# Kernel optimization log

Hardware: AMD Instinct MI355X
Metric: run time of the kernel (lower is better)

## Reference

```python
import jax, jax.numpy as jnp
import numpy as np

S, H, E, DFF = 8192, 1024, 8, 4096
CAPACITY = (S * 1) // E  # capacity_factor=1.0, k=1 -> 1024 (>= min_capacity 4)


def setup_inputs() -> dict:
    key = jax.random.key(0)
    ks = jax.random.split(key, 6)
    sc_in = 1.0 / np.sqrt(H)
    sc_ff = 1.0 / np.sqrt(DFF)
    return {
        "hidden_states": jax.random.normal(ks[0], (S, H), dtype=jnp.float32),
        "wg": jax.random.normal(ks[1], (H, E), dtype=jnp.float32) * sc_in,
        "w1": jax.random.normal(ks[2], (E, H, DFF), dtype=jnp.float32) * sc_in,
        "b1": jnp.zeros((E, DFF), dtype=jnp.float32),
        "w2": jax.random.normal(ks[3], (E, DFF, H), dtype=jnp.float32) * sc_ff,
        "b2": jnp.zeros((E, H), dtype=jnp.float32),
    }


def _top1_gate(x, wg):
    # DeepSpeed top1gating (noisy_gate_policy=None, used_token=None)
    logits = x @ wg                                   # [S, E]
    gates = jax.nn.softmax(logits, axis=-1)           # [S, E]
    idx = jnp.argmax(gates, axis=-1)                  # [S]
    mask1 = jax.nn.one_hot(idx, E, dtype=gates.dtype) # [S, E]
    # load-balancing aux loss (uses pre-capacity mask)
    me = jnp.mean(gates, axis=0)
    ce = jnp.mean(mask1, axis=0)
    l_aux = jnp.sum(me * ce) * E
    # capacity-based token dropping
    locations1 = jnp.cumsum(mask1, axis=0) - 1.0      # position within expert
    mask1 = mask1 * (locations1 < CAPACITY)
    exp_counts = jnp.sum(mask1, axis=0).astype(jnp.int32)
    loc_s = jnp.sum(locations1 * mask1, axis=1).astype(jnp.int32)   # [S]
    loc_sc = jax.nn.one_hot(loc_s, CAPACITY, dtype=gates.dtype)     # [S, C]
    combine = jnp.einsum("se,sc->sec", gates * mask1, loc_sc)       # [S, E, C]
    dispatch = (combine > 0).astype(gates.dtype)
    return l_aux, combine, dispatch, exp_counts


def reference(hidden_states, wg, w1, b1, w2, b2):
    l_aux, combine, dispatch, exp_counts = _top1_gate(hidden_states, wg)
    # dispatch tokens to expert slots: [E, C, H]
    disp = jnp.einsum("sec,sh->ech", dispatch, hidden_states)
    # grouped expert FFN (GELU MLP)
    h1 = jax.nn.gelu(jnp.einsum("ech,ehf->ecf", disp, w1) + b1[:, None, :])
    eo = jnp.einsum("ecf,efh->ech", h1, w2) + b2[:, None, :]
    # combine back to token order, weighted by gate values
    out = jnp.einsum("sec,ech->sh", combine, eo)      # [S, H]
    # dropout prob = 0.0 -> identity
    return out, l_aux, exp_counts
```

## Files before the change

kernel.cpp:

```cpp
#include <hip/hip_runtime.h>

#define S_TOK 8192
#define H_DIM 1024
#define NE    8
#define CAP   1024
#define DFF   4096

typedef unsigned short u16;
typedef __bf16 bf16_t;
typedef bf16_t bf16x8 __attribute__((ext_vector_type(8)));
typedef float  f32x4  __attribute__((ext_vector_type(4)));

__device__ __forceinline__ u16 f2bf(float f) {
  union { float f; unsigned u; } a; a.f = f;
  unsigned u = a.u;
  u += 0x7fffu + ((u >> 16) & 1u);
  return (u16)(u >> 16);
}

__device__ __forceinline__ float gelu_tanh(float x) {
  const float c = 0.7978845608028654f;
  float t = tanhf(c * (x + 0.044715f * x * x * x));
  return 0.5f * x * (1.0f + t);
}

__global__ void gate_kernel(const float* __restrict__ x, const float* __restrict__ wg,
                            float* __restrict__ gate, int* __restrict__ expert,
                            int* __restrict__ rank, int* __restrict__ blockCnt,
                            float* __restrict__ blockMe) {
  __shared__ float sg[16][8];
  __shared__ int   se[16];
  int tid = threadIdx.x, lane = tid & 63, w = tid >> 6;
  int b = blockIdx.x;
  for (int j = 0; j < 4; ++j) {
    int t = w * 4 + j;
    int s = b * 16 + t;
    const float* xr = x + (size_t)s * H_DIM;
    float acc[8];
#pragma unroll
    for (int e = 0; e < 8; ++e) acc[e] = 0.f;
#pragma unroll
    for (int i = 0; i < 16; ++i) {
      int h = i * 64 + lane;
      float xv = xr[h];
      float4 wa = *(const float4*)(wg + h * 8);
      float4 wb = *(const float4*)(wg + h * 8 + 4);
      acc[0] += xv * wa.x; acc[1] += xv * wa.y; acc[2] += xv * wa.z; acc[3] += xv * wa.w;
      acc[4] += xv * wb.x; acc[5] += xv * wb.y; acc[6] += xv * wb.z; acc[7] += xv * wb.w;
    }
#pragma unroll
    for (int off = 32; off >= 1; off >>= 1)
#pragma unroll
      for (int e = 0; e < 8; ++e) acc[e] += __shfl_down(acc[e], off);
    if (lane == 0) {
      float mx = acc[0];
#pragma unroll
      for (int e = 1; e < 8; ++e) mx = fmaxf(mx, acc[e]);
      float g[8], Z = 0.f;
#pragma unroll
      for (int e = 0; e < 8; ++e) { g[e] = expf(acc[e] - mx); Z += g[e]; }
      int am = 0; float best = acc[0];
#pragma unroll
      for (int e = 1; e < 8; ++e) if (acc[e] > best) { best = acc[e]; am = e; }
      float inv = 1.f / Z;
#pragma unroll
      for (int e = 0; e < 8; ++e) sg[t][e] = g[e] * inv;
      se[t] = am;
      gate[s] = g[am] * inv;
      expert[s] = am;
    }
  }
  __syncthreads();
  if (tid < 16) {
    int e = se[tid], r = 0;
    for (int t2 = 0; t2 < tid; ++t2) r += (se[t2] == e) ? 1 : 0;
    rank[b * 16 + tid] = r;
  }
  if (tid < 8) {
    int c = 0; float m = 0.f;
#pragma unroll
    for (int t = 0; t < 16; ++t) { c += (se[t] == tid) ? 1 : 0; m += sg[t][tid]; }
    blockCnt[b * 8 + tid] = c;
    blockMe[b * 8 + tid] = m;
  }
}

__global__ void scan_kernel(const int* __restrict__ blockCnt, const float* __restrict__ blockMe,
                            int* __restrict__ blockOff, int* __restrict__ counts,
                            float* __restrict__ tail) {
  int tid = threadIdx.x;
  int e = tid >> 6, lane = tid & 63;
  int run = 0; float msum = 0.f;
  for (int c = 0; c < 8; ++c) {
    int b = c * 64 + lane;
    int v = blockCnt[b * 8 + e];
    float mv = blockMe[b * 8 + e];
    int sc = v;
#pragma unroll
    for (int off = 1; off < 64; off <<= 1) {
      int u = __shfl_up(sc, off);
      if (lane >= off) sc += u;
    }
    blockOff[b * 8 + e] = run + sc - v;
    run += __shfl(sc, 63);
#pragma unroll
    for (int off = 32; off >= 1; off >>= 1) mv += __shfl_down(mv, off);
    msum += __shfl(mv, 0);
  }
  __shared__ float sm[8];
  __shared__ int scnt[8];
  if (lane == 0) {
    sm[e] = msum; scnt[e] = run;
    counts[e] = run < CAP ? run : CAP;
  }
  __syncthreads();
  if (tid == 0) {
    float la = 0.f;
    for (int i = 0; i < 8; ++i)
      la += (sm[i] / (float)S_TOK) * ((float)scnt[i] / (float)S_TOK);
    tail[0] = la * (float)NE;
    for (int i = 0; i < 8; ++i) {
      int cc = scnt[i] < CAP ? scnt[i] : CAP;
      tail[1 + i] = (float)cc;
    }
  }
}

__global__ void assign_kernel(const int* __restrict__ expert, const int* __restrict__ rank,
                              const int* __restrict__ blockOff, int* __restrict__ slot_token) {
  int s = blockIdx.x * 256 + threadIdx.x;
  int e = expert[s];
  int pos = blockOff[(s >> 4) * 8 + e] + rank[s];
  if (pos < CAP) slot_token[e * CAP + pos] = s;
}

__global__ void gather_kernel(const float* __restrict__ x, const int* __restrict__ slot_token,
                              const int* __restrict__ counts, u16* __restrict__ disp) {
  int slot = blockIdx.x;
  int e = slot >> 10, c = slot & 1023;
  int t = threadIdx.x;
  ushort4 v4;
  if (c < counts[e]) {
    int s = slot_token[slot];
    float4 v = *(const float4*)(x + (size_t)s * H_DIM + t * 4);
    v4.x = f2bf(v.x); v4.y = f2bf(v.y); v4.z = f2bf(v.z); v4.w = f2bf(v.w);
  } else {
    v4.x = 0; v4.y = 0; v4.z = 0; v4.w = 0;
  }
  *(ushort4*)(disp + (size_t)slot * H_DIM + t * 4) = v4;
}

__global__ void transpose_convert(const float* __restrict__ src0, u16* __restrict__ dst0,
                                  int R, int C) {
  __shared__ float tile[64][65];
  int e = blockIdx.z;
  const float* src = src0 + (size_t)e * R * C;
  u16* dst = dst0 + (size_t)e * R * C;
  int c0 = blockIdx.x * 64, r0 = blockIdx.y * 64;
  int g = threadIdx.x & 15, rr = threadIdx.x >> 4;
#pragma unroll
  for (int p = 0; p < 4; ++p) {
    int r = rr + p * 16;
    float4 v = *(const float4*)(src + (size_t)(r0 + r) * C + c0 + g * 4);
    tile[r][g * 4 + 0] = v.x;
    tile[r][g * 4 + 1] = v.y;
    tile[r][g * 4 + 2] = v.z;
    tile[r][g * 4 + 3] = v.w;
  }
  __syncthreads();
#pragma unroll
  for (int p = 0; p < 4; ++p) {
    int c = rr + p * 16;
    ushort4 o;
    o.x = f2bf(tile[g * 4 + 0][c]);
    o.y = f2bf(tile[g * 4 + 1][c]);
    o.z = f2bf(tile[g * 4 + 2][c]);
    o.w = f2bf(tile[g * 4 + 3][c]);
    *(ushort4*)(dst + (size_t)(c0 + c) * R + r0 + g * 4) = o;
  }
}

__global__ __launch_bounds__(256, 2) void gemm1_kernel(const u16* __restrict__ disp,
                                                       const u16* __restrict__ w1t,
                                                       const float* __restrict__ b1,
                                                       u16* __restrict__ h1) {
  __shared__ __align__(16) u16 As[2][8192];
  __shared__ __align__(16) u16 Bs[2][8192];
  int flat = blockIdx.x;
  int swz = (flat & 7) * 256 + (flat >> 3);
  int e  = swz >> 8;
  int r  = swz & 255;
  int bx = r >> 3;
  int by = r & 7;
  int m0 = by * 128, n0 = bx * 128;
  const u16* A  = disp + (size_t)e * CAP * H_DIM + (size_t)m0 * H_DIM;
  const u16* Bt = w1t + (size_t)e * DFF * H_DIM + (size_t)n0 * H_DIM;

  int tid = threadIdx.x, lane = tid & 63, w = tid >> 6;
  int wm = w >> 1, wn = w & 1, q = lane >> 4, l15 = lane & 15;

  const u16* gpA[4]; const u16* gpB[4]; int lofs[4];
#pragma unroll
  for (int i = 0; i < 4; ++i) {
    int p = (w * 4 + i) * 64 + lane;
    int row = p >> 3, slot = p & 7;
    int kq = slot ^ (row & 7);
    gpA[i] = A + (size_t)row * H_DIM + kq * 8;
    gpB[i] = Bt + (size_t)row * H_DIM + kq * 8;
    lofs[i] = (w * 4 + i) * 512;
  }

  int aoff[2][4], boff[2][4];
#pragma unroll
  for (int t = 0; t < 4; ++t) {
    int ra = wm * 64 + t * 16 + l15;
    int rb = wn * 64 + t * 16 + l15;
#pragma unroll
    for (int s = 0; s < 2; ++s) {
      aoff[s][t] = ra * 64 + (((s * 4) + q) ^ (ra & 7)) * 8;
      boff[s][t] = rb * 64 + (((s * 4) + q) ^ (rb & 7)) * 8;
    }
  }

  f32x4 acc[4][4];
  f32x4 zero = {0.f, 0.f, 0.f, 0.f};
#pragma unroll
  for (int i = 0; i < 4; ++i)
#pragma unroll
    for (int j = 0; j < 4; ++j) acc[i][j] = zero;

#pragma unroll
  for (int i = 0; i < 4; ++i) {
    __builtin_amdgcn_global_load_lds((__attribute__((address_space(1))) int*)(gpA[i]),
                                     (__attribute__((address_space(3))) int*)(&As[0][0] + lofs[i]), 16, 0, 0);
    __builtin_amdgcn_global_load_lds((__attribute__((address_space(1))) int*)(gpB[i]),
                                     (__attribute__((address_space(3))) int*)(&Bs[0][0] + lofs[i]), 16, 0, 0);
  }
  __syncthreads();

  int cur = 0;
  for (int kt = 0; kt < H_DIM; kt += 64) {
    if (kt + 64 < H_DIM) {
      int nxt = cur ^ 1;
#pragma unroll
      for (int i = 0; i < 4; ++i) {
        __builtin_amdgcn_global_load_lds((__attribute__((address_space(1))) int*)(gpA[i] + kt + 64),
                                         (__attribute__((address_space(3))) int*)(&As[nxt][0] + lofs[i]), 16, 0, 0);
        __builtin_amdgcn_global_load_lds((__attribute__((address_space(1))) int*)(gpB[i] + kt + 64),
                                         (__attribute__((address_space(3))) int*)(&Bs[nxt][0] + lofs[i]), 16, 0, 0);
      }
    }
#pragma unroll
    for (int s = 0; s < 2; ++s) {
      bf16x8 af[4], bfr[4];
#pragma unroll
      for (int t = 0; t < 4; ++t) af[t] = *(const bf16x8*)(&As[cur][0] + aoff[s][t]);
#pragma unroll
      for (int t = 0; t < 4; ++t) bfr[t] = *(const bf16x8*)(&Bs[cur][0] + boff[s][t]);
#pragma unroll
      for (int mt = 0; mt < 4; ++mt)
#pragma unroll
        for (int nt = 0; nt < 4; ++nt)
          acc[mt][nt] = __builtin_amdgcn_mfma_f32_16x16x32_bf16(af[mt], bfr[nt], acc[mt][nt], 0, 0, 0);
    }
    __syncthreads();
    cur ^= 1;
  }

  const float* b1e = b1 + e * DFF;
  u16* out = h1 + (size_t)e * CAP * DFF;
#pragma unroll
  for (int mt = 0; mt < 4; ++mt)
#pragma unroll
    for (int nt = 0; nt < 4; ++nt) {
      int col = n0 + wn * 64 + nt * 16 + l15;
      float bias = b1e[col];
#pragma unroll
      for (int rr = 0; rr < 4; ++rr) {
        int row = m0 + wm * 64 + mt * 16 + q * 4 + rr;
        out[(size_t)row * DFF + col] = f2bf(gelu_tanh(acc[mt][nt][rr] + bias));
      }
    }
}

__global__ __launch_bounds__(512, 4) void gemm2_kernel(const u16* __restrict__ h1,
                                                       const u16* __restrict__ w2t,
                                                       const float* __restrict__ b2,
                                                       const int* __restrict__ slot_token,
                                                       const float* __restrict__ gate,
                                                       const int* __restrict__ counts,
                                                       float* __restrict__ out) {
  __shared__ __align__(16) u16 As[2][8192];
  __shared__ __align__(16) u16 Bs[2][8192];
  int flat = blockIdx.x;
  int swz = (flat & 7) * 64 + (flat >> 3);
  int e  = swz >> 6;
  int r  = swz & 63;
  int bx = r & 7;
  int by = r >> 3;
  int m0 = by * 128, n0 = bx * 128;
  const u16* A  = h1 + (size_t)e * CAP * DFF + (size_t)m0 * DFF;
  const u16* Bt = w2t + (size_t)e * H_DIM * DFF + (size_t)n0 * DFF;
  int tid = threadIdx.x, lane = tid & 63, w = tid >> 6;
  int wm = w >> 2, wn = w & 3;
  int q = lane >> 4, l15 = lane & 15;
  f32x4 acc[4][2];
  f32x4 zero = {0.f, 0.f, 0.f, 0.f};
#pragma unroll
  for (int i = 0; i < 4; ++i) { acc[i][0] = zero; acc[i][1] = zero; }

  const u16* gsrc = (w < 4) ? A : Bt;
  int isA = (w < 4) ? 1 : 0;
  int q4 = w & 3;
  const u16* gp[4]; int lofs[4];
#pragma unroll
  for (int i = 0; i < 4; ++i) {
    int p = (q4 * 4 + i) * 64 + lane;
    int row = p >> 3, slot = p & 7;
    int kq = slot ^ (row & 7);
    gp[i] = gsrc + (size_t)row * DFF + kq * 8;
    lofs[i] = (q4 * 4 + i) * 512;
  }

  int aoff[2][4], boff[2][2];
#pragma unroll
  for (int t = 0; t < 4; ++t) {
    int ra = wm * 64 + t * 16 + l15;
#pragma unroll
    for (int s = 0; s < 2; ++s)
      aoff[s][t] = ra * 64 + (((s * 4) + q) ^ (ra & 7)) * 8;
  }
#pragma unroll
  for (int t = 0; t < 2; ++t) {
    int rb = wn * 32 + t * 16 + l15;
#pragma unroll
    for (int s = 0; s < 2; ++s)
      boff[s][t] = rb * 64 + (((s * 4) + q) ^ (rb & 7)) * 8;
  }

  {
    u16* sb = isA ? &As[0][0] : &Bs[0][0];
#pragma unroll
    for (int i = 0; i < 4; ++i)
      __builtin_amdgcn_global_load_lds((__attribute__((address_space(1))) int*)(gp[i]),
                                       (__attribute__((address_space(3))) int*)(sb + lofs[i]), 16, 0, 0);
  }
  __syncthreads();

  int cur = 0;
  for (int kt = 0; kt < DFF; kt += 64) {
    if (kt + 64 < DFF) {
      int nxt = cur ^ 1;
      u16* sb = isA ? &As[nxt][0] : &Bs[nxt][0];
#pragma unroll
      for (int i = 0; i < 4; ++i)
        __builtin_amdgcn_global_load_lds((__attribute__((address_space(1))) int*)(gp[i] + kt + 64),
                                         (__attribute__((address_space(3))) int*)(sb + lofs[i]), 16, 0, 0);
    }
#pragma unroll
    for (int s = 0; s < 2; ++s) {
      bf16x8 af[4], bfr[2];
#pragma unroll
      for (int t = 0; t < 4; ++t) af[t] = *(const bf16x8*)(&As[cur][0] + aoff[s][t]);
#pragma unroll
      for (int t = 0; t < 2; ++t) bfr[t] = *(const bf16x8*)(&Bs[cur][0] + boff[s][t]);
#pragma unroll
      for (int mt = 0; mt < 4; ++mt)
#pragma unroll
        for (int nt = 0; nt < 2; ++nt)
          acc[mt][nt] = __builtin_amdgcn_mfma_f32_16x16x32_bf16(af[mt], bfr[nt], acc[mt][nt], 0, 0, 0);
    }
    __syncthreads();
    cur ^= 1;
  }

  int cnt = counts[e];
  const float* b2e = b2 + e * H_DIM;
#pragma unroll
  for (int mt = 0; mt < 4; ++mt) {
    int tok[4]; float gv[4];
#pragma unroll
    for (int rr = 0; rr < 4; ++rr) {
      int c = m0 + wm * 64 + mt * 16 + q * 4 + rr;
      if (c < cnt) { int s = slot_token[e * CAP + c]; tok[rr] = s; gv[rr] = gate[s]; }
      else { tok[rr] = -1; gv[rr] = 0.f; }
    }
#pragma unroll
    for (int nt = 0; nt < 2; ++nt) {
      int col = n0 + wn * 32 + nt * 16 + l15;
      float bias = b2e[col];
#pragma unroll
      for (int rr = 0; rr < 4; ++rr)
        if (tok[rr] >= 0)
          out[(size_t)tok[rr] * H_DIM + col] = gv[rr] * (acc[mt][nt][rr] + bias);
    }
  }
}

extern "C" void kernel_launch(void* const* d_in, const int* in_sizes, int n_in,
                              void* d_out, int out_size, void* d_ws, size_t ws_size,
                              hipStream_t stream) {
  const float* x  = (const float*)d_in[0];
  const float* wg = (const float*)d_in[1];
  const float* w1 = (const float*)d_in[2];
  const float* b1 = (const float*)d_in[3];
  const float* w2 = (const float*)d_in[4];
  const float* b2 = (const float*)d_in[5];
  float* out = (float*)d_out;
  char* ws = (char*)d_ws;
  const size_t MB = 1024 * 1024;
  u16* w1t  = (u16*)(ws);
  u16* w2t  = (u16*)(ws + 64 * MB);
  u16* disp = (u16*)(ws + 128 * MB);
  u16* h1   = (u16*)(ws + 144 * MB);
  char* sm = ws + 208 * MB;
  float* gate      = (float*)(sm);
  int*   expert    = (int*)(sm + 32 * 1024);
  int*   rank      = (int*)(sm + 64 * 1024);
  int*   slot_tok  = (int*)(sm + 96 * 1024);
  int*   blockCnt  = (int*)(sm + 128 * 1024);
  int*   blockOff  = (int*)(sm + 144 * 1024);
  float* blockMe   = (float*)(sm + 160 * 1024);
  int*   counts    = (int*)(sm + 176 * 1024);

  hipMemsetAsync(d_out, 0, (size_t)out_size * sizeof(float), stream);
  gate_kernel<<<512, 256, 0, stream>>>(x, wg, gate, expert, rank, blockCnt, blockMe);
  scan_kernel<<<1, 512, 0, stream>>>(blockCnt, blockMe, blockOff, counts,
                                     out + (size_t)S_TOK * H_DIM);
  assign_kernel<<<32, 256, 0, stream>>>(expert, rank, blockOff, slot_tok);
  gather_kernel<<<8192, 256, 0, stream>>>(x, slot_tok, counts, disp);
  transpose_convert<<<dim3(DFF / 64, H_DIM / 64, NE), 256, 0, stream>>>(w1, w1t, H_DIM, DFF);
  transpose_convert<<<dim3(H_DIM / 64, DFF / 64, NE), 256, 0, stream>>>(w2, w2t, DFF, H_DIM);
  gemm1_kernel<<<2048, 256, 0, stream>>>(disp, w1t, b1, h1);
  gemm2_kernel<<<512, 512, 0, stream>>>(h1, w2t, b2, slot_tok, gate, counts, out);
}
```

Baseline: 610.6 us.

## Single-buffer LDS in expert GEMMs to raise occupancy; use exp-based GELU

Both expert GEMM kernels drop LDS double buffering and switch to a single buffer with load, sync, compute, sync per K step. This halves shared memory per block, and gemm1's launch bounds are raised so more blocks fit per CU, relying on inter-block parallelism to hide memory latency instead of in-block prefetch. The tanh GELU is rewritten as x*sigmoid(2u) using a fast exp and a hardware reciprocal, which is mathematically equivalent but has slightly different rounding. The risk is that global load latency is now exposed within each block if occupancy does not make up for the lost prefetch.

After: 578.7 us. -5.2%, faster.

```diff
diff --git a/kernel.cpp b/kernel.cpp
--- a/kernel.cpp
+++ b/kernel.cpp
@@ -18,10 +18,10 @@
   return (u16)(u >> 16);
 }
 
-__device__ __forceinline__ float gelu_tanh(float x) {
-  const float c = 0.7978845608028654f;
-  float t = tanhf(c * (x + 0.044715f * x * x * x));
-  return 0.5f * x * (1.0f + t);
+__device__ __forceinline__ float gelu_fast(float x) {
+  float u = 1.5957691216057308f * x * (1.0f + 0.044715f * x * x);
+  float ez = __expf(-u);
+  return x * __builtin_amdgcn_rcpf(1.0f + ez);
 }
 
 __global__ void gate_kernel(const float* __restrict__ x, const float* __restrict__ wg,
@@ -180,12 +180,12 @@
   }
 }
 
-__global__ __launch_bounds__(256, 2) void gemm1_kernel(const u16* __restrict__ disp,
+__global__ __launch_bounds__(256, 3) void gemm1_kernel(const u16* __restrict__ disp,
                                                        const u16* __restrict__ w1t,
                                                        const float* __restrict__ b1,
                                                        u16* __restrict__ h1) {
-  __shared__ __align__(16) u16 As[2][8192];
-  __shared__ __align__(16) u16 Bs[2][8192];
+  __shared__ __align__(16) u16 As[8192];
+  __shared__ __align__(16) u16 Bs[8192];
   int flat = blockIdx.x;
   int swz = (flat & 7) * 256 + (flat >> 3);
   int e  = swz >> 8;
@@ -229,34 +229,22 @@
 #pragma unroll
     for (int j = 0; j < 4; ++j) acc[i][j] = zero;
 
-#pragma unroll
-  for (int i = 0; i < 4; ++i) {
-    __builtin_amdgcn_global_load_lds((__attribute__((address_space(1))) int*)(gpA[i]),
-                                     (__attribute__((address_space(3))) int*)(&As[0][0] + lofs[i]), 16, 0, 0);
-    __builtin_amdgcn_global_load_lds((__attribute__((address_space(1))) int*)(gpB[i]),
-                                     (__attribute__((address_space(3))) int*)(&Bs[0][0] + lofs[i]), 16, 0, 0);
-  }
-  __syncthreads();
-
-  int cur = 0;
   for (int kt = 0; kt < H_DIM; kt += 64) {
-    if (kt + 64 < H_DIM) {
-      int nxt = cur ^ 1;
-#pragma unroll
-      for (int i = 0; i < 4; ++i) {
-        __builtin_amdgcn_global_load_lds((__attribute__((address_space(1))) int*)(gpA[i] + kt + 64),
-                                         (__attribute__((address_space(3))) int*)(&As[nxt][0] + lofs[i]), 16, 0, 0);
-        __builtin_amdgcn_global_load_lds((__attribute__((address_space(1))) int*)(gpB[i] + kt + 64),
-                                         (__attribute__((address_space(3))) int*)(&Bs[nxt][0] + lofs[i]), 16, 0, 0);
-      }
-    }
+#pragma unroll
+    for (int i = 0; i < 4; ++i) {
+      __builtin_amdgcn_global_load_lds((__attribute__((address_space(1))) int*)(gpA[i] + kt),
+                                       (__attribute__((address_space(3))) int*)(As + lofs[i]), 16, 0, 0);
+      __builtin_amdgcn_global_load_lds((__attribute__((address_space(1))) int*)(gpB[i] + kt),
+                                       (__attribute__((address_space(3))) int*)(Bs + lofs[i]), 16, 0, 0);
+    }
+    __syncthreads();
 #pragma unroll
     for (int s = 0; s < 2; ++s) {
       bf16x8 af[4], bfr[4];
 #pragma unroll
-      for (int t = 0; t < 4; ++t) af[t] = *(const bf16x8*)(&As[cur][0] + aoff[s][t]);
-#pragma unroll
-      for (int t = 0; t < 4; ++t) bfr[t] = *(const bf16x8*)(&Bs[cur][0] + boff[s][t]);
+      for (int t = 0; t < 4; ++t) af[t] = *(const bf16x8*)(As + aoff[s][t]);
+#pragma unroll
+      for (int t = 0; t < 4; ++t) bfr[t] = *(const bf16x8*)(Bs + boff[s][t]);
 #pragma unroll
       for (int mt = 0; mt < 4; ++mt)
 #pragma unroll
@@ -264,7 +252,6 @@
           acc[mt][nt] = __builtin_amdgcn_mfma_f32_16x16x32_bf16(af[mt], bfr[nt], acc[mt][nt], 0, 0, 0);
     }
     __syncthreads();
-    cur ^= 1;
   }
 
   const float* b1e = b1 + e * DFF;
@@ -278,7 +265,7 @@
 #pragma unroll
       for (int rr = 0; rr < 4; ++rr) {
         int row = m0 + wm * 64 + mt * 16 + q * 4 + rr;
-        out[(size_t)row * DFF + col] = f2bf(gelu_tanh(acc[mt][nt][rr] + bias));
+        out[(size_t)row * DFF + col] = f2bf(gelu_fast(acc[mt][nt][rr] + bias));
       }
     }
 }
@@ -290,8 +277,8 @@
                                                        const float* __restrict__ gate,
                                                        const int* __restrict__ counts,
                                                        float* __restrict__ out) {
-  __shared__ __align__(16) u16 As[2][8192];
-  __shared__ __align__(16) u16 Bs[2][8192];
+  __shared__ __align__(16) u16 As[8192];
+  __shared__ __align__(16) u16 Bs[8192];
   int flat = blockIdx.x;
   int swz = (flat & 7) * 64 + (flat >> 3);
   int e  = swz >> 6;
@@ -310,7 +297,7 @@
   for (int i = 0; i < 4; ++i) { acc[i][0] = zero; acc[i][1] = zero; }
 
   const u16* gsrc = (w < 4) ? A : Bt;
-  int isA = (w < 4) ? 1 : 0;
+  u16* ldst = (w < 4) ? As : Bs;
   int q4 = w & 3;
   const u16* gp[4]; int lofs[4];
 #pragma unroll
@@ -338,32 +325,19 @@
       boff[s][t] = rb * 64 + (((s * 4) + q) ^ (rb & 7)) * 8;
   }
 
-  {
-    u16* sb = isA ? &As[0][0] : &Bs[0][0];
+  for (int kt = 0; kt < DFF; kt += 64) {
 #pragma unroll
     for (int i = 0; i < 4; ++i)
-      __builtin_amdgcn_global_load_lds((__attribute__((address_space(1))) int*)(gp[i]),
-                                       (__attribute__((address_space(3))) int*)(sb + lofs[i]), 16, 0, 0);
-  }
-  __syncthreads();
-
-  int cur = 0;
-  for (int kt = 0; kt < DFF; kt += 64) {
-    if (kt + 64 < DFF) {
-      int nxt = cur ^ 1;
-      u16* sb = isA ? &As[nxt][0] : &Bs[nxt][0];
-#pragma unroll
-      for (int i = 0; i < 4; ++i)
-        __builtin_amdgcn_global_load_lds((__attribute__((address_space(1))) int*)(gp[i] + kt + 64),
-                                         (__attribute__((address_space(3))) int*)(sb + lofs[i]), 16, 0, 0);
-    }
+      __builtin_amdgcn_global_load_lds((__attribute__((address_space(1))) int*)(gp[i] + kt),
+                                       (__attribute__((address_space(3))) int*)(ldst + lofs[i]), 16, 0, 0);
+    __syncthreads();
 #pragma unroll
     for (int s = 0; s < 2; ++s) {
       bf16x8 af[4], bfr[2];
 #pragma unroll
-      for (int t = 0; t < 4; ++t) af[t] = *(const bf16x8*)(&As[cur][0] + aoff[s][t]);
-#pragma unroll
-      for (int t = 0; t < 2; ++t) bfr[t] = *(const bf16x8*)(&Bs[cur][0] + boff[s][t]);
+      for (int t = 0; t < 4; ++t) af[t] = *(const bf16x8*)(As + aoff[s][t]);
+#pragma unroll
+      for (int t = 0; t < 2; ++t) bfr[t] = *(const bf16x8*)(Bs + boff[s][t]);
 #pragma unroll
       for (int mt = 0; mt < 4; ++mt)
 #pragma unroll
@@ -371,7 +345,6 @@
           acc[mt][nt] = __builtin_amdgcn_mfma_f32_16x16x32_bf16(af[mt], bfr[nt], acc[mt][nt], 0, 0, 0);
     }
     __syncthreads();
-    cur ^= 1;
   }
 
   int cnt = counts[e];
```
